# Optimization experiments

Measured on AMD Instinct MI355X. Metric: run time of the kernel, lower is better.

Reference implementation:

```python
import jax, jax.numpy as jnp
import numpy as np

B, N, NS, D, H = 32, 4096, 16, 512, 8
DH = D // H          # dims_per_head = 64
DFF = 4 * D          # ff_mlp hidden
SCALE = DH ** -0.5
EPS = 1e-8           # slot-attention renorm eps
LN_EPS = 1e-5        # torch LayerNorm default
ITERS = 3


def layer_norm(x, g, b):
    mu = jnp.mean(x, axis=-1, keepdims=True)
    var = jnp.mean((x - mu) ** 2, axis=-1, keepdims=True)
    return (x - mu) * jax.lax.rsqrt(var + LN_EPS) * g + b


def setup_inputs() -> dict:
    key = jax.random.key(0)
    ks = jax.random.split(key, 8)
    s = 0.02
    return {
        "inputs": jax.random.normal(ks[0], (B, N, D), jnp.float32),
        "conditioning": jax.random.normal(ks[1], (B, NS, D), jnp.float32),
        # norm_input
        "ln_in_g": jnp.ones((D,), jnp.float32),
        "ln_in_b": jnp.zeros((D,), jnp.float32),
        # projections (no bias: use_projection_bias=False)
        "Wk": jax.random.normal(ks[2], (D, D), jnp.float32) * s,
        "Wv": jax.random.normal(ks[3], (D, D), jnp.float32) * s,
        "Wq": jax.random.normal(ks[4], (D, D), jnp.float32) * s,
        "Wo": jax.random.normal(ks[5], (D, D), jnp.float32) * s,
        # norm_slots / norm_slots_ff_mlp
        "ln_s_g": jnp.ones((D,), jnp.float32),
        "ln_s_b": jnp.zeros((D,), jnp.float32),
        "ln_f_g": jnp.ones((D,), jnp.float32),
        "ln_f_b": jnp.zeros((D,), jnp.float32),
        # ff_mlp: Linear(D,4D) -> ReLU -> Linear(4D,D)
        "W1": jax.random.normal(ks[6], (D, DFF), jnp.float32) * s,
        "b1": jnp.zeros((DFF,), jnp.float32),
        "W2": jax.random.normal(ks[7], (DFF, D), jnp.float32) * s,
        "b2": jnp.zeros((D,), jnp.float32),
    }


def reference(inputs, conditioning, ln_in_g, ln_in_b, Wk, Wv, Wq, Wo,
              ln_s_g, ln_s_b, ln_f_g, ln_f_b, W1, b1, W2, b2):
    b = inputs.shape[0]
    x = layer_norm(inputs, ln_in_g, ln_in_b)                 # [b, n, D]
    k = (x @ Wk.T).reshape(b, N, H, DH)                      # [b, n, h, dh]
    v = (x @ Wv.T).reshape(b, N, H, DH)

    slots = conditioning
    attn_mean = None
    for _ in range(ITERS):
        slots_prev = slots
        s = layer_norm(slots, ln_s_g, ln_s_b)
        q = (s @ Wq.T).reshape(b, NS, H, DH)                 # [b, ns, h, dh]
        dots = jnp.einsum("bihd,bjhd->bihj", q, k) * SCALE   # [b, ns, h, n]
        # softmax over flattened (slots, heads) axis, per input location j
        attn = jax.nn.softmax(dots.reshape(b, NS * H, N), axis=1)
        attn = attn.reshape(b, NS, H, N)
        attn_before = attn
        attn = attn + EPS
        attn = attn / jnp.sum(attn, axis=-1, keepdims=True)  # renorm over j
        updates = jnp.einsum("bjhd,bihj->bihd", v, attn)     # [b, ns, h, dh]
        updates = updates.reshape(b, NS, D)
        slots = updates @ Wo.T + slots_prev                  # to_o + residual
        slots_prev_ff = slots
        s2 = layer_norm(slots, ln_f_g, ln_f_b)
        s2 = jax.nn.relu(s2 @ W1 + b1) @ W2 + b2             # ff_mlp
        slots = s2 + slots_prev_ff
        attn_mean = jnp.mean(attn_before, axis=2)            # [b, ns, n]
    return slots, attn_mean
```

## Files before the change

kernel.cpp:

```cpp
#include <hip/hip_runtime.h>
#include <cstdint>
#include <cstddef>

typedef __attribute__((ext_vector_type(8))) short short8;
typedef __attribute__((ext_vector_type(4))) short short4v;
typedef __attribute__((ext_vector_type(8))) __bf16 bf16x8;
typedef __attribute__((ext_vector_type(4))) float f32x4;
typedef unsigned short u16;

static constexpr int Bb = 32, Nn = 4096, NSs = 16, Dd = 512, Hh = 8, DFF = 2048;
static constexpr float SCALE = 0.125f;
static constexpr float EPSR  = 1e-8f;
static constexpr float LN_EPS = 1e-5f;

__device__ __forceinline__ u16 f2b(float x) {
  union { float f; uint32_t u; } a; a.f = x;
  uint32_t r = a.u + 0x7fffu + ((a.u >> 16) & 1u);
  return (u16)(r >> 16);
}

__device__ __forceinline__ f32x4 mfma16(short8 a, short8 b, f32x4 c) {
  return __builtin_amdgcn_mfma_f32_16x16x32_bf16(
      __builtin_bit_cast(bf16x8, a), __builtin_bit_cast(bf16x8, b), c, 0, 0, 0);
}

__device__ __forceinline__ void gload16(const u16* g, u16* l) {
  __builtin_amdgcn_global_load_lds(
      (const __attribute__((address_space(1))) void*)g,
      (__attribute__((address_space(3))) void*)l, 16, 0, 0);
}

__global__ __launch_bounds__(256) void ln_rows(const float* __restrict__ src,
    const float* __restrict__ g, const float* __restrict__ bt,
    u16* __restrict__ dst, int R) {
  int row = blockIdx.x * 4 + (threadIdx.x >> 6);
  if (row >= R) return;
  int lane = threadIdx.x & 63;
  const float* p = src + (size_t)row * Dd + lane * 8;
  float4 u0 = *(const float4*)p;
  float4 u1 = *(const float4*)(p + 4);
  float x[8] = {u0.x,u0.y,u0.z,u0.w,u1.x,u1.y,u1.z,u1.w};
  float s = 0.f, s2 = 0.f;
#pragma unroll
  for (int e = 0; e < 8; ++e) { s += x[e]; s2 += x[e]*x[e]; }
#pragma unroll
  for (int m = 1; m < 64; m <<= 1) { s += __shfl_xor(s, m); s2 += __shfl_xor(s2, m); }
  float mean = s * (1.f/512.f);
  float var  = s2 * (1.f/512.f) - mean*mean;
  float rstd = rsqrtf(var + LN_EPS);
  union { u16 o[8]; short8 v; } ou;
#pragma unroll
  for (int e = 0; e < 8; ++e)
    ou.o[e] = f2b((x[e]-mean)*rstd*g[lane*8+e] + bt[lane*8+e]);
  *(short8*)(dst + (size_t)row * Dd + lane * 8) = ou.v;
}

template<int EP>
__global__ __launch_bounds__(256) void gemm_bt(const u16* __restrict__ A,
    const u16* __restrict__ Bw, void* __restrict__ Cp,
    const float* __restrict__ bias, const float* __restrict__ res,
    int N, int K) {
  __shared__ u16 lA[128*32];
  __shared__ u16 lB[128*32];
  const int tid = threadIdx.x, lane = tid & 63, wid = tid >> 6;
  const int wr = wid >> 1, wc = wid & 1;
  const int bm = blockIdx.y * 128, bn = blockIdx.x * 128;
  f32x4 acc[4][4] = {};
  const int srow = wid*16 + (lane >> 2), scol = (lane & 3) * 8;
  const u16* Ap = A + (size_t)(bm + srow) * K + scol;
  const u16* Bp = Bw + (size_t)(bn + srow) * K + scol;
  u16* lAd = &lA[wid * 512];
  u16* lBd = &lB[wid * 512];
  const int li = lane & 15, lk = lane >> 4;
  for (int k0 = 0; k0 < K; k0 += 32) {
    __syncthreads();
    gload16(Ap + k0, lAd);
    gload16(Ap + (size_t)64*K + k0, lAd + 2048);
    gload16(Bp + k0, lBd);
    gload16(Bp + (size_t)64*K + k0, lBd + 2048);
    __syncthreads();
    short8 af[4], bf[4];
#pragma unroll
    for (int m = 0; m < 4; ++m)
      af[m] = *(const short8*)&lA[(wr*64 + m*16 + li)*32 + lk*8];
#pragma unroll
    for (int n = 0; n < 4; ++n)
      bf[n] = *(const short8*)&lB[(wc*64 + n*16 + li)*32 + lk*8];
#pragma unroll
    for (int m = 0; m < 4; ++m)
#pragma unroll
      for (int n = 0; n < 4; ++n)
        acc[m][n] = mfma16(af[m], bf[n], acc[m][n]);
  }
  const int lr = lk * 4;
#pragma unroll
  for (int m = 0; m < 4; ++m)
#pragma unroll
    for (int n = 0; n < 4; ++n) {
      int row = bm + wr*64 + m*16 + lr;
      int col = bn + wc*64 + n*16 + li;
      f32x4 v = acc[m][n];
#pragma unroll
      for (int r = 0; r < 4; ++r) {
        size_t off = (size_t)(row + r) * N + col;
        float x = v[r];
        if constexpr (EP == 0) ((u16*)Cp)[off] = f2b(x);
        else if constexpr (EP == 1) ((float*)Cp)[off] = x + res[off];
        else if constexpr (EP == 2) { x += bias[col]; ((u16*)Cp)[off] = f2b(x > 0.f ? x : 0.f); }
        else ((float*)Cp)[off] = x + bias[col] + res[off];
      }
    }
}

template<int EP>
__global__ __launch_bounds__(256) void gemm64(const u16* __restrict__ A,
    const u16* __restrict__ Bw, void* __restrict__ Cp,
    const float* __restrict__ bias, const float* __restrict__ res,
    int N, int K) {
  __shared__ u16 lA[64*32];
  __shared__ u16 lB[64*32];
  const int tid = threadIdx.x, lane = tid & 63, wid = tid >> 6;
  const int wr = wid >> 1, wc = wid & 1;
  const int bm = blockIdx.y * 64, bn = blockIdx.x * 64;
  f32x4 acc[2][2] = {};
  const int srow = wid*16 + (lane >> 2), scol = (lane & 3) * 8;
  const u16* Ap = A + (size_t)(bm + srow) * K + scol;
  const u16* Bp = Bw + (size_t)(bn + srow) * K + scol;
  u16* lAd = &lA[wid * 512];
  u16* lBd = &lB[wid * 512];
  const int li = lane & 15, lk = lane >> 4;
  for (int k0 = 0; k0 < K; k0 += 32) {
    __syncthreads();
    gload16(Ap + k0, lAd);
    gload16(Bp + k0, lBd);
    __syncthreads();
    short8 af[2], bf[2];
#pragma unroll
    for (int m = 0; m < 2; ++m)
      af[m] = *(const short8*)&lA[(wr*32 + m*16 + li)*32 + lk*8];
#pragma unroll
    for (int n = 0; n < 2; ++n)
      bf[n] = *(const short8*)&lB[(wc*32 + n*16 + li)*32 + lk*8];
#pragma unroll
    for (int m = 0; m < 2; ++m)
#pragma unroll
      for (int n = 0; n < 2; ++n)
        acc[m][n] = mfma16(af[m], bf[n], acc[m][n]);
  }
  const int lr = lk * 4;
#pragma unroll
  for (int m = 0; m < 2; ++m)
#pragma unroll
    for (int n = 0; n < 2; ++n) {
      int row = bm + wr*32 + m*16 + lr;
      int col = bn + wc*32 + n*16 + li;
      f32x4 v = acc[m][n];
#pragma unroll
      for (int r = 0; r < 4; ++r) {
        size_t off = (size_t)(row + r) * N + col;
        float x = v[r];
        if constexpr (EP == 0) ((u16*)Cp)[off] = f2b(x);
        else if constexpr (EP == 1) ((float*)Cp)[off] = x + res[off];
        else if constexpr (EP == 2) { x += bias[col]; ((u16*)Cp)[off] = f2b(x > 0.f ? x : 0.f); }
        else ((float*)Cp)[off] = x + bias[col] + res[off];
      }
    }
}

__global__ __launch_bounds__(256) void attn_a(const u16* __restrict__ q,
    const u16* __restrict__ kk, u16* __restrict__ attnb,
    float* __restrict__ rowsum, float* __restrict__ attn_mean) {
  const int jt = blockIdx.x, b = blockIdx.y;
  const int tid = threadIdx.x, lane = tid & 63, wid = tid >> 6;
  __shared__ float sc[64][129];
  __shared__ float red[4][64];
  const int li = lane & 15, lk = lane >> 4;
#pragma unroll
  for (int hh = 0; hh < 2; ++hh) {
    const int h = wid * 2 + hh;
    const u16* qb = q + (((size_t)b*16 + li)*8 + h)*64 + lk*8;
    short8 a0 = *(const short8*)qb;
    short8 a1 = *(const short8*)(qb + 32);
#pragma unroll
    for (int n = 0; n < 4; ++n) {
      const u16* kb = kk + ((size_t)b*Nn + jt*64 + n*16 + li)*Dd + h*64 + lk*8;
      f32x4 acc = {};
      acc = mfma16(a0, *(const short8*)kb, acc);
      acc = mfma16(a1, *(const short8*)(kb + 32), acc);
#pragma unroll
      for (int r = 0; r < 4; ++r)
        sc[n*16 + li][(lk*4 + r)*8 + h] = acc[r] * SCALE;
    }
  }
  __syncthreads();
  const int jl = tid & 63, qt = tid >> 6;
  float mx = -1e30f;
#pragma unroll
  for (int e = 0; e < 32; ++e) mx = fmaxf(mx, sc[jl][qt*32 + e]);
  red[qt][jl] = mx;
  __syncthreads();
  float M = fmaxf(fmaxf(red[0][jl], red[1][jl]), fmaxf(red[2][jl], red[3][jl]));
  __syncthreads();
  float s = 0.f;
#pragma unroll
  for (int e = 0; e < 32; ++e) {
    float ev = __expf(sc[jl][qt*32 + e] - M);
    sc[jl][qt*32 + e] = ev; s += ev;
  }
  red[qt][jl] = s;
  __syncthreads();
  float S = red[0][jl] + red[1][jl] + red[2][jl] + red[3][jl];
  float inv = 1.f / S;
#pragma unroll
  for (int e = 0; e < 32; ++e)
    sc[jl][qt*32 + e] = sc[jl][qt*32 + e] * inv + EPSR;
  __syncthreads();
  if (tid < 128) {
    float rs = 0.f;
    for (int j2 = 0; j2 < 64; ++j2) rs += sc[j2][tid];
    atomicAdd(&rowsum[b*128 + tid], rs);
  }
#pragma unroll
  for (int e = 0; e < 32; ++e) {
    int r = qt*32 + e;
    attnb[((size_t)b*128 + r)*Nn + jt*64 + jl] = f2b(sc[jl][r]);
  }
  if (attn_mean != nullptr && tid < 64) {
    for (int i = 0; i < 16; ++i) {
      float sm = 0.f;
#pragma unroll
      for (int h = 0; h < 8; ++h) sm += sc[tid][i*8 + h];
      attn_mean[((size_t)b*16 + i)*Nn + jt*64 + tid] = sm * 0.125f - EPSR;
    }
  }
}

__global__ __launch_bounds__(256) void attn_b(const u16* __restrict__ attnb,
    const u16* __restrict__ vT, const float* __restrict__ rowsum,
    u16* __restrict__ upd) {
  const int h = blockIdx.x, b = blockIdx.y;
  const int lane = threadIdx.x & 63, wid = threadIdx.x >> 6;
  const int li = lane & 15, lk = lane >> 4;
  const size_t BN = (size_t)Bb * Nn;
  const u16* Ap = attnb + ((size_t)b*128 + li*8 + h)*Nn + lk*8;
  const u16* Bp = vT + (size_t)(h*64 + wid*16 + li)*BN + (size_t)b*Nn + lk*8;
  f32x4 acc[4] = {};
  for (int k0 = 0; k0 < Nn; k0 += 128) {
#pragma unroll
    for (int e = 0; e < 4; ++e)
      acc[e] = mfma16(*(const short8*)(Ap + k0 + e*32),
                      *(const short8*)(Bp + k0 + e*32), acc[e]);
  }
#pragma unroll
  for (int r = 0; r < 4; ++r) {
    int i = lk*4 + r;
    float t = acc[0][r] + acc[1][r] + acc[2][r] + acc[3][r];
    float rs = rowsum[b*128 + i*8 + h];
    upd[((size_t)b*16 + i)*Dd + h*64 + wid*16 + li] = f2b(t / rs);
  }
}

__global__ void cvt_w(const float* __restrict__ s, u16* __restrict__ d, int n) {
  int i = blockIdx.x*256 + threadIdx.x;
  if (i < n) d[i] = f2b(s[i]);
}
__global__ __launch_bounds__(256) void tr_cvt(const float* __restrict__ s,
    u16* __restrict__ d, int R, int C) {
  __shared__ u16 t[32][33];
  const int c0 = blockIdx.x*32, r0 = blockIdx.y*32;
  const int tr = threadIdx.x >> 3, tc4 = (threadIdx.x & 7)*4;
  float4 v = *(const float4*)&s[(size_t)(r0+tr)*C + c0 + tc4];
  t[tr][tc4+0] = f2b(v.x); t[tr][tc4+1] = f2b(v.y);
  t[tr][tc4+2] = f2b(v.z); t[tr][tc4+3] = f2b(v.w);
  __syncthreads();
  const int oc = threadIdx.x >> 3, or4 = (threadIdx.x & 7)*4;
  union { u16 o[4]; short4v v4; } ou;
#pragma unroll
  for (int e = 0; e < 4; ++e) ou.o[e] = t[or4+e][oc];
  *(short4v*)&d[(size_t)(c0+oc)*R + r0 + or4] = ou.v4;
}
__global__ void copy_f32v4(const float* __restrict__ s, float* __restrict__ d, int n4) {
  int i = blockIdx.x*256 + threadIdx.x;
  if (i < n4) ((float4*)d)[i] = ((const float4*)s)[i];
}

extern "C" void kernel_launch(void* const* d_in, const int* in_sizes, int n_in,
                              void* d_out, int out_size, void* d_ws, size_t ws_size,
                              hipStream_t stream) {
  (void)in_sizes; (void)n_in; (void)out_size; (void)ws_size;
  const float* inputs  = (const float*)d_in[0];
  const float* cond    = (const float*)d_in[1];
  const float* ln_in_g = (const float*)d_in[2];
  const float* ln_in_b = (const float*)d_in[3];
  const float* Wk = (const float*)d_in[4];
  const float* Wv = (const float*)d_in[5];
  const float* Wq = (const float*)d_in[6];
  const float* Wo = (const float*)d_in[7];
  const float* ln_s_g = (const float*)d_in[8];
  const float* ln_s_b = (const float*)d_in[9];
  const float* ln_f_g = (const float*)d_in[10];
  const float* ln_f_b = (const float*)d_in[11];
  const float* W1 = (const float*)d_in[12];
  const float* b1 = (const float*)d_in[13];
  const float* W2 = (const float*)d_in[14];
  const float* b2 = (const float*)d_in[15];
  float* out_slots = (float*)d_out;
  float* out_amean = (float*)d_out + (size_t)Bb*NSs*Dd;

  char* w = (char*)d_ws;
  auto alloc = [&](size_t bytes) {
    char* p = w; w += (bytes + 255) & ~(size_t)255; return p;
  };
  u16*  xn    = (u16*)alloc((size_t)Bb*Nn*Dd*2);
  u16*  kbuf  = (u16*)alloc((size_t)Bb*Nn*Dd*2);
  u16*  vT    = (u16*)alloc((size_t)Bb*Nn*Dd*2);
  u16*  attnb = (u16*)alloc((size_t)Bb*128*Nn*2);
  float* slots = (float*)alloc((size_t)Bb*NSs*Dd*4);
  u16*  qb    = (u16*)alloc((size_t)Bb*NSs*Dd*2);
  u16*  snb   = (u16*)alloc((size_t)Bb*NSs*Dd*2);
  u16*  s2nb  = (u16*)alloc((size_t)Bb*NSs*Dd*2);
  u16*  h1b   = (u16*)alloc((size_t)Bb*NSs*DFF*2);
  u16*  updb  = (u16*)alloc((size_t)Bb*NSs*Dd*2);
  float* rowsum = (float*)alloc((size_t)Bb*128*3*4);
  u16*  wkb = (u16*)alloc(262144*2);
  u16*  wvb = (u16*)alloc(262144*2);
  u16*  wqb = (u16*)alloc(262144*2);
  u16*  wob = (u16*)alloc(262144*2);
  u16*  w1t = (u16*)alloc((size_t)1048576*2);
  u16*  w2t = (u16*)alloc((size_t)1048576*2);

  cvt_w<<<1024, 256, 0, stream>>>(Wk, wkb, 262144);
  cvt_w<<<1024, 256, 0, stream>>>(Wv, wvb, 262144);
  cvt_w<<<1024, 256, 0, stream>>>(Wq, wqb, 262144);
  cvt_w<<<1024, 256, 0, stream>>>(Wo, wob, 262144);
  tr_cvt<<<dim3(64, 16), 256, 0, stream>>>(W1, w1t, 512, 2048);
  tr_cvt<<<dim3(16, 64), 256, 0, stream>>>(W2, w2t, 2048, 512);
  copy_f32v4<<<256, 256, 0, stream>>>(cond, slots, 65536);
  hipMemsetAsync(rowsum, 0, (size_t)Bb*128*3*4, stream);
  ln_rows<<<Bb*Nn/4, 256, 0, stream>>>(inputs, ln_in_g, ln_in_b, xn, Bb*Nn);
  gemm_bt<0><<<dim3(4, Bb*Nn/128), 256, 0, stream>>>(xn, wkb, kbuf, nullptr, nullptr, 512, 512);
  gemm_bt<0><<<dim3(Bb*Nn/128, 4), 256, 0, stream>>>(wvb, xn, vT, nullptr, nullptr, Bb*Nn, 512);

  for (int it = 0; it < 3; ++it) {
    float* rs = rowsum + (size_t)it * Bb * 128;
    ln_rows<<<128, 256, 0, stream>>>(slots, ln_s_g, ln_s_b, snb, Bb*NSs);
    gemm64<0><<<dim3(8, 8), 256, 0, stream>>>(snb, wqb, qb, nullptr, nullptr, 512, 512);
    attn_a<<<dim3(Nn/64, Bb), 256, 0, stream>>>(qb, kbuf, attnb, rs,
                                                it == 2 ? out_amean : nullptr);
    attn_b<<<dim3(Hh, Bb), 256, 0, stream>>>(attnb, vT, rs, updb);
    gemm64<1><<<dim3(8, 8), 256, 0, stream>>>(updb, wob, slots, nullptr, slots, 512, 512);
    ln_rows<<<128, 256, 0, stream>>>(slots, ln_f_g, ln_f_b, s2nb, Bb*NSs);
    gemm64<2><<<dim3(32, 8), 256, 0, stream>>>(s2nb, w1t, h1b, b1, nullptr, 2048, 512);
    gemm64<3><<<dim3(8, 8), 256, 0, stream>>>(h1b, w2t, slots, b2, slots, 512, 2048);
  }
  copy_f32v4<<<256, 256, 0, stream>>>(slots, out_slots, 65536);
}
```

Baseline: 744.6 us.

## Fuse K and V projection GEMMs into one kernel sharing the input tile

Replaces the two separate K and V projection GEMMs with one kernel that loads each normalized-input tile once and multiplies it against both Wk and Wv tiles, writing K row-major and V transposed with a packed 4-element store. This removes a second full read of the large normalized input and one kernel launch. In exchange it doubles the accumulator registers per thread (two 4x4 MFMA accumulator sets), adds shared memory for the third tile and requests two blocks per CU, which may cause spills or lower occupancy. The transposed V store is now strided across rows.

```diff
diff --git a/kernel.cpp b/kernel.cpp
--- a/kernel.cpp
+++ b/kernel.cpp
@@ -55,42 +55,51 @@
   *(short8*)(dst + (size_t)row * Dd + lane * 8) = ou.v;
 }
 
-template<int EP>
-__global__ __launch_bounds__(256) void gemm_bt(const u16* __restrict__ A,
-    const u16* __restrict__ Bw, void* __restrict__ Cp,
-    const float* __restrict__ bias, const float* __restrict__ res,
-    int N, int K) {
+__global__ __launch_bounds__(256, 2) void gemm_kv(const u16* __restrict__ A,
+    const u16* __restrict__ Bk, const u16* __restrict__ Bv,
+    u16* __restrict__ Ck, u16* __restrict__ CvT) {
   __shared__ u16 lA[128*32];
-  __shared__ u16 lB[128*32];
+  __shared__ u16 lK[128*32];
+  __shared__ u16 lV[128*32];
   const int tid = threadIdx.x, lane = tid & 63, wid = tid >> 6;
   const int wr = wid >> 1, wc = wid & 1;
   const int bm = blockIdx.y * 128, bn = blockIdx.x * 128;
-  f32x4 acc[4][4] = {};
+  const size_t BN = (size_t)Bb * Nn;
+  f32x4 ak[4][4] = {};
+  f32x4 av[4][4] = {};
   const int srow = wid*16 + (lane >> 2), scol = (lane & 3) * 8;
-  const u16* Ap = A + (size_t)(bm + srow) * K + scol;
-  const u16* Bp = Bw + (size_t)(bn + srow) * K + scol;
+  const u16* Ap = A  + (size_t)(bm + srow) * Dd + scol;
+  const u16* Kp = Bk + (size_t)(bn + srow) * Dd + scol;
+  const u16* Vp = Bv + (size_t)(bn + srow) * Dd + scol;
   u16* lAd = &lA[wid * 512];
-  u16* lBd = &lB[wid * 512];
+  u16* lKd = &lK[wid * 512];
+  u16* lVd = &lV[wid * 512];
   const int li = lane & 15, lk = lane >> 4;
-  for (int k0 = 0; k0 < K; k0 += 32) {
+  for (int k0 = 0; k0 < Dd; k0 += 32) {
     __syncthreads();
     gload16(Ap + k0, lAd);
-    gload16(Ap + (size_t)64*K + k0, lAd + 2048);
-    gload16(Bp + k0, lBd);
-    gload16(Bp + (size_t)64*K + k0, lBd + 2048);
+    gload16(Ap + (size_t)64*Dd + k0, lAd + 2048);
+    gload16(Kp + k0, lKd);
+    gload16(Kp + (size_t)64*Dd + k0, lKd + 2048);
+    gload16(Vp + k0, lVd);
+    gload16(Vp + (size_t)64*Dd + k0, lVd + 2048);
     __syncthreads();
-    short8 af[4], bf[4];
+    short8 af[4], kf[4], vf[4];
 #pragma unroll
     for (int m = 0; m < 4; ++m)
       af[m] = *(const short8*)&lA[(wr*64 + m*16 + li)*32 + lk*8];
 #pragma unroll
-    for (int n = 0; n < 4; ++n)
-      bf[n] = *(const short8*)&lB[(wc*64 + n*16 + li)*32 + lk*8];
+    for (int n = 0; n < 4; ++n) {
+      kf[n] = *(const short8*)&lK[(wc*64 + n*16 + li)*32 + lk*8];
+      vf[n] = *(const short8*)&lV[(wc*64 + n*16 + li)*32 + lk*8];
+    }
 #pragma unroll
     for (int m = 0; m < 4; ++m)
 #pragma unroll
-      for (int n = 0; n < 4; ++n)
-        acc[m][n] = mfma16(af[m], bf[n], acc[m][n]);
+      for (int n = 0; n < 4; ++n) {
+        ak[m][n] = mfma16(af[m], kf[n], ak[m][n]);
+        av[m][n] = mfma16(af[m], vf[n], av[m][n]);
+      }
   }
   const int lr = lk * 4;
 #pragma unroll
@@ -99,16 +108,15 @@
     for (int n = 0; n < 4; ++n) {
       int row = bm + wr*64 + m*16 + lr;
       int col = bn + wc*64 + n*16 + li;
-      f32x4 v = acc[m][n];
-#pragma unroll
-      for (int r = 0; r < 4; ++r) {
-        size_t off = (size_t)(row + r) * N + col;
-        float x = v[r];
-        if constexpr (EP == 0) ((u16*)Cp)[off] = f2b(x);
-        else if constexpr (EP == 1) ((float*)Cp)[off] = x + res[off];
-        else if constexpr (EP == 2) { x += bias[col]; ((u16*)Cp)[off] = f2b(x > 0.f ? x : 0.f); }
-        else ((float*)Cp)[off] = x + bias[col] + res[off];
-      }
+      f32x4 vk = ak[m][n];
+#pragma unroll
+      for (int r = 0; r < 4; ++r)
+        Ck[(size_t)(row + r) * Dd + col] = f2b(vk[r]);
+      f32x4 vv = av[m][n];
+      union { u16 o[4]; short4v v4; } ou;
+#pragma unroll
+      for (int r = 0; r < 4; ++r) ou.o[r] = f2b(vv[r]);
+      *(short4v*)&CvT[(size_t)col * BN + row] = ou.v4;
     }
 }
 
@@ -338,8 +346,7 @@
   copy_f32v4<<<256, 256, 0, stream>>>(cond, slots, 65536);
   hipMemsetAsync(rowsum, 0, (size_t)Bb*128*3*4, stream);
   ln_rows<<<Bb*Nn/4, 256, 0, stream>>>(inputs, ln_in_g, ln_in_b, xn, Bb*Nn);
-  gemm_bt<0><<<dim3(4, Bb*Nn/128), 256, 0, stream>>>(xn, wkb, kbuf, nullptr, nullptr, 512, 512);
-  gemm_bt<0><<<dim3(Bb*Nn/128, 4), 256, 0, stream>>>(wvb, xn, vT, nullptr, nullptr, Bb*Nn, 512);
+  gemm_kv<<<dim3(4, Bb*Nn/128), 256, 0, stream>>>(xn, wkb, wvb, kbuf, vT);
 
   for (int it = 0; it < 3; ++it) {
     float* rs = rowsum + (size_t)it * Bb * 128;
```

Measured after the change: 726.7 us. -2.4%, faster.
